# Kernel tuning notes

Measured on AMD Instinct MI355X. Metric: run time of the kernel, lower is better.

## Reference

```python
import jax, jax.numpy as jnp
import numpy as np

INPUT_DIM = 1024
OUTPUT_DIM = 1024
DOWN = INPUT_DIM // 8  # reduction_factor=8
NUM_TOKENS = 2


def setup_inputs() -> dict:
    key = jax.random.key(0)
    k1, k2, k3, k4, k5 = jax.random.split(key, 5)
    B, Sx, Sy = 32, 2048, 512
    x = jax.random.normal(k1, (B, Sx, INPUT_DIM), dtype=jnp.float32)
    y = jax.random.normal(k2, (B, Sy, INPUT_DIM), dtype=jnp.float32)
    # nn.Parameter(torch.rand(...)) -> uniform [0,1)
    latent_tokens = jax.random.uniform(k3, (NUM_TOKENS, INPUT_DIM), dtype=jnp.float32)
    gate = jnp.zeros((1,), dtype=jnp.float32)
    # Conv1d kernel_size=1, no bias == pointwise matmul; kaiming-uniform-ish init
    lim_d = 1.0 / np.sqrt(INPUT_DIM)
    lim_u = 1.0 / np.sqrt(DOWN)
    W_down = jax.random.uniform(k4, (DOWN, INPUT_DIM), dtype=jnp.float32, minval=-lim_d, maxval=lim_d)
    W_up = jax.random.uniform(k5, (OUTPUT_DIM, DOWN), dtype=jnp.float32, minval=-lim_u, maxval=lim_u)
    return {"x": x, "y": y, "latent_tokens": latent_tokens, "gate": gate,
            "W_down": W_down, "W_up": W_up}


def reference(x, y, latent_tokens, gate, W_down, W_up):
    # tokens attend over y:  [B,T,Sy] softmax over Sy
    att_y2t = jax.nn.softmax(jnp.einsum('td,bsd->bts', latent_tokens, y), axis=-1)
    tokens = latent_tokens[None] + jnp.einsum('bts,bsd->btd', att_y2t, y)  # [B,T,D]
    # x attends over tokens: [B,Sx,T] softmax over T
    att_t2x = jax.nn.softmax(jnp.einsum('bsd,btd->bst', x, tokens), axis=-1)
    x_res = jnp.einsum('bst,btd->bsd', att_t2x, tokens)
    x = x + gate * x_res
    # 1x1 conv bottleneck: down -> ReLU -> up (pointwise matmuls)
    z = jax.nn.relu(jnp.einsum('bsd,ed->bse', x, W_down))
    out = jnp.einsum('bse,oe->bso', z, W_up)
    return out
```

## Files before the change

### kernel.cpp

```cpp
#include <hip/hip_runtime.h>
#include <hip/hip_bf16.h>

#define B_N 32
#define SX 2048
#define SY 512
#define DIM 1024
#define NTOK 2
#define DN 128
#define ODIM 1024
#define BM 64
#define KH 512

typedef __bf16 bf16;
typedef __bf16 bf16x8 __attribute__((ext_vector_type(8)));
typedef __bf16 bf16x4 __attribute__((ext_vector_type(4)));
typedef float f32x4 __attribute__((ext_vector_type(4)));

__device__ __forceinline__ f32x4 mfma16(bf16x8 a, bf16x8 b, f32x4 c) {
  return __builtin_amdgcn_mfma_f32_16x16x32_bf16(a, b, c, 0, 0, 0);
}

__global__ __launch_bounds__(256) void prep_kernel(const float* __restrict__ Wd,
                                                   const float* __restrict__ Wu,
                                                   bf16* __restrict__ wdb,
                                                   bf16* __restrict__ wub) {
  int i = blockIdx.x * 256 + threadIdx.x;
  if (i < DN * DIM) {
    wdb[i] = (bf16)Wd[i];
    wub[i] = (bf16)Wu[i];
  }
}

__global__ __launch_bounds__(256) void tokens_kernel(const float* __restrict__ y,
                                                     const float* __restrict__ lat,
                                                     const float* __restrict__ gate,
                                                     float* __restrict__ tokens) {
  if (gate[0] == 0.0f) return;
  __shared__ float s_lat[NTOK][DIM];
  __shared__ float s_sc[NTOK][SY];
  int b = blockIdx.x;
  int tid = threadIdx.x, wave = tid >> 6, lane = tid & 63;
  const float* yb = y + (size_t)b * SY * DIM;
  for (int i = tid; i < NTOK * DIM; i += 256) ((float*)s_lat)[i] = lat[i];
  __syncthreads();
  for (int s = wave * 128; s < wave * 128 + 128; ++s) {
    const float* yr = yb + (size_t)s * DIM;
    float d0 = 0.f, d1 = 0.f;
#pragma unroll
    for (int i = 0; i < 4; ++i) {
      f32x4 v = *(const f32x4*)(yr + lane * 4 + i * 256);
      f32x4 l0 = *(const f32x4*)(&s_lat[0][lane * 4 + i * 256]);
      f32x4 l1 = *(const f32x4*)(&s_lat[1][lane * 4 + i * 256]);
      d0 += v[0] * l0[0] + v[1] * l0[1] + v[2] * l0[2] + v[3] * l0[3];
      d1 += v[0] * l1[0] + v[1] * l1[1] + v[2] * l1[2] + v[3] * l1[3];
    }
#pragma unroll
    for (int off = 32; off > 0; off >>= 1) {
      d0 += __shfl_xor(d0, off);
      d1 += __shfl_xor(d1, off);
    }
    if (lane == 0) { s_sc[0][s] = d0; s_sc[1][s] = d1; }
  }
  __syncthreads();
  if (wave < 2) {
    float m = -3.4e38f;
    for (int s = lane; s < SY; s += 64) m = fmaxf(m, s_sc[wave][s]);
#pragma unroll
    for (int off = 32; off > 0; off >>= 1) m = fmaxf(m, __shfl_xor(m, off));
    float sum = 0.f;
    for (int s = lane; s < SY; s += 64) {
      float e = expf(s_sc[wave][s] - m);
      s_sc[wave][s] = e;
      sum += e;
    }
#pragma unroll
    for (int off = 32; off > 0; off >>= 1) sum += __shfl_xor(sum, off);
    float inv = 1.f / sum;
    for (int s = lane; s < SY; s += 64) s_sc[wave][s] *= inv;
  }
  __syncthreads();
  float a0[4] = {0.f, 0.f, 0.f, 0.f}, a1[4] = {0.f, 0.f, 0.f, 0.f};
  for (int s = 0; s < SY; ++s) {
    float p0 = s_sc[0][s], p1 = s_sc[1][s];
    const float* yr = yb + (size_t)s * DIM;
#pragma unroll
    for (int i = 0; i < 4; ++i) {
      float v = yr[tid + i * 256];
      a0[i] += p0 * v;
      a1[i] += p1 * v;
    }
  }
  float* tb = tokens + (size_t)b * NTOK * DIM;
#pragma unroll
  for (int i = 0; i < 4; ++i) {
    tb[tid + i * 256] = s_lat[0][tid + i * 256] + a0[i];
    tb[DIM + tid + i * 256] = s_lat[1][tid + i * 256] + a1[i];
  }
}

__global__ __launch_bounds__(256) void xprime_kernel(const float* __restrict__ x,
                                                     const float* __restrict__ gate,
                                                     const float* __restrict__ tokens,
                                                     float* __restrict__ xp) {
  float g = gate[0];
  if (g == 0.0f) return;
  __shared__ float s_tok[NTOK][DIM];
  __shared__ float s_c[BM][2];
  int tid = threadIdx.x, w = tid >> 6, lane = tid & 63;
  size_t m0 = (size_t)blockIdx.x * BM;
  int b = (int)(m0 / SX);
  const float* xb = x + m0 * DIM;
  const float* tokb = tokens + (size_t)b * NTOK * DIM;
  for (int i = tid; i < NTOK * DIM; i += 256) ((float*)s_tok)[i] = tokb[i];
  __syncthreads();
  for (int i = 0; i < 16; ++i) {
    int r = w * 16 + i;
    const float* xrow = xb + (size_t)r * DIM;
    float d0 = 0.f, d1 = 0.f;
#pragma unroll
    for (int c = 0; c < 4; ++c) {
      f32x4 v = *(const f32x4*)(xrow + lane * 4 + c * 256);
      f32x4 t0 = *(const f32x4*)(&s_tok[0][lane * 4 + c * 256]);
      f32x4 t1 = *(const f32x4*)(&s_tok[1][lane * 4 + c * 256]);
      d0 += v[0] * t0[0] + v[1] * t0[1] + v[2] * t0[2] + v[3] * t0[3];
      d1 += v[0] * t1[0] + v[1] * t1[1] + v[2] * t1[2] + v[3] * t1[3];
    }
#pragma unroll
    for (int off = 32; off > 0; off >>= 1) {
      d0 += __shfl_xor(d0, off);
      d1 += __shfl_xor(d1, off);
    }
    if (lane == 0) {
      float mm = fmaxf(d0, d1);
      float e0 = expf(d0 - mm), e1 = expf(d1 - mm);
      float inv = g / (e0 + e1);
      s_c[r][0] = e0 * inv;
      s_c[r][1] = e1 * inv;
    }
  }
  __syncthreads();
  float* xpb = xp + m0 * DIM;
  for (int r = w * 16; r < w * 16 + 16; ++r) {
    float c0 = s_c[r][0], c1 = s_c[r][1];
#pragma unroll
    for (int c = 0; c < 4; ++c) {
      f32x4 v = *(const f32x4*)(xb + (size_t)r * DIM + lane * 4 + c * 256);
      f32x4 t0 = *(const f32x4*)(&s_tok[0][lane * 4 + c * 256]);
      f32x4 t1 = *(const f32x4*)(&s_tok[1][lane * 4 + c * 256]);
      f32x4 o;
#pragma unroll
      for (int j = 0; j < 4; ++j) o[j] = v[j] + c0 * t0[j] + c1 * t1[j];
      *(f32x4*)(xpb + (size_t)r * DIM + lane * 4 + c * 256) = o;
    }
  }
}

__global__ __launch_bounds__(512, 4) void main_kernel(const float* __restrict__ x,
                                                      const float* __restrict__ gate,
                                                      const float* __restrict__ xp,
                                                      const bf16* __restrict__ wdb,
                                                      const bf16* __restrict__ wub,
                                                      float* __restrict__ out) {
  __shared__ bf16 xs[BM * KH];
  __shared__ bf16 zsm[BM * DN];

  int tid = threadIdx.x, w = tid >> 6, lane = tid & 63;
  int lq = lane >> 4, lr = lane & 15;
  size_t m0 = (size_t)blockIdx.x * BM;
  float g = gate[0];
  const float* xb = ((g != 0.f) ? xp : x) + m0 * DIM;

  char* xls = (char*)xs;
  char* zls = (char*)zsm;

  f32x4 acc[4] = {};

  auto LOADH = [&](int h) {
    f32x4 xv[8][2];
#pragma unroll
    for (int i = 0; i < 8; ++i) {
      int row = w + i * 8;
      const float* p = xb + (size_t)row * DIM + h * KH + lane * 8;
      xv[i][0] = *(const f32x4*)p;
      xv[i][1] = *(const f32x4*)(p + 4);
    }
#pragma unroll
    for (int i = 0; i < 8; ++i) {
      int row = w + i * 8;
      bf16x8 o;
#pragma unroll
      for (int j = 0; j < 4; ++j) {
        o[j] = (bf16)xv[i][0][j];
        o[4 + j] = (bf16)xv[i][1][j];
      }
      *(bf16x8*)(xls + row * (KH * 2) + ((lane * 16) ^ (w << 4))) = o;
    }
  };

  auto COMPH = [&](int h) {
    const bf16* wdw = wdb + (size_t)(w * 16 + lr) * DIM + h * KH + lq * 8;
#pragma unroll 4
    for (int kc = 0; kc < KH / 32; ++kc) {
      bf16x8 wf = *(const bf16x8*)(wdw + kc * 32);
#pragma unroll
      for (int mt = 0; mt < 4; ++mt) {
        int xr = mt * 16 + lr;
        bf16x8 xf = *(const bf16x8*)(xls + xr * (KH * 2) +
                                     (((kc * 32 + lq * 8) * 2) ^ ((xr & 7) << 4)));
        acc[mt] = mfma16(wf, xf, acc[mt]);
      }
    }
  };

  LOADH(0);
  __syncthreads();
  COMPH(0);
  __syncthreads();
  LOADH(1);
  __syncthreads();
  COMPH(1);

#pragma unroll
  for (int mt = 0; mt < 4; ++mt) {
    int xr = mt * 16 + lr;
    int dn = w * 16 + lq * 4;
    bf16x4 pk;
#pragma unroll
    for (int r = 0; r < 4; ++r) pk[r] = (bf16)fmaxf(acc[mt][r], 0.f);
    *(bf16x4*)(zls + xr * (DN * 2) + ((dn * 2) ^ ((xr & 7) << 4))) = pk;
  }
  __syncthreads();

  bf16x8 zF[4][4];
#pragma unroll
  for (int mt = 0; mt < 4; ++mt)
#pragma unroll
    for (int kt = 0; kt < 4; ++kt) {
      int xr = mt * 16 + lr;
      zF[kt][mt] = *(const bf16x8*)(zls + xr * (DN * 2) +
                                    (((kt * 32 + lq * 8) * 2) ^ ((xr & 7) << 4)));
    }

  float* ob = out + m0 * ODIM;
#pragma unroll 2
  for (int oc16 = 0; oc16 < 8; ++oc16) {
    int base = w * 128 + oc16 * 16;
    bf16x8 wu[4];
#pragma unroll
    for (int kt = 0; kt < 4; ++kt)
      wu[kt] = *(const bf16x8*)(wub + (size_t)(base + lr) * DN + kt * 32 + lq * 8);
    f32x4 a2[4] = {};
#pragma unroll
    for (int kt = 0; kt < 4; ++kt)
#pragma unroll
      for (int mt = 0; mt < 4; ++mt)
        a2[mt] = mfma16(wu[kt], zF[kt][mt], a2[mt]);
#pragma unroll
    for (int mt = 0; mt < 4; ++mt)
      *(f32x4*)(ob + (size_t)(mt * 16 + lr) * ODIM + base + lq * 4) = a2[mt];
  }
}

extern "C" void kernel_launch(void* const* d_in, const int* in_sizes, int n_in,
                              void* d_out, int out_size, void* d_ws, size_t ws_size,
                              hipStream_t stream) {
  const float* x = (const float*)d_in[0];
  const float* y = (const float*)d_in[1];
  const float* lat = (const float*)d_in[2];
  const float* gate = (const float*)d_in[3];
  const float* Wd = (const float*)d_in[4];
  const float* Wu = (const float*)d_in[5];
  float* out = (float*)d_out;
  char* ws = (char*)d_ws;

  float* tokens = (float*)ws;
  bf16* wdb = (bf16*)(ws + 262144);
  bf16* wub = (bf16*)(ws + 524288);

  prep_kernel<<<(DN * DIM + 255) / 256, 256, 0, stream>>>(Wd, Wu, wdb, wub);
  tokens_kernel<<<B_N, 256, 0, stream>>>(y, lat, gate, tokens);
  xprime_kernel<<<(B_N * SX) / BM, 256, 0, stream>>>(x, gate, tokens, out);
  main_kernel<<<(B_N * SX) / BM, 512, 0, stream>>>(x, gate, out, wdb, wub, out);
}
```

Before: 162.6 us.

## Double-buffer x tiles in LDS and prefetch next K-quarter into registers

Splits the down-projection K loop into four 256-wide quarters with two LDS buffers. Global loads of the next x quarter and the W_down fragments are issued into registers before the MFMAs on the current buffer run, so load latency overlaps compute. The old scheme loaded half of K, synced, then computed with no overlap. The cost is more registers for the prefetched data, extra barriers per quarter, and a rewritten LDS swizzle that the read and write sides must agree on.

```diff
diff --git a/kernel.cpp b/kernel.cpp
--- a/kernel.cpp
+++ b/kernel.cpp
@@ -9,7 +9,8 @@
 #define DN 128
 #define ODIM 1024
 #define BM 64
-#define KH 512
+#define QK 256
+#define NQ 4
 
 typedef __bf16 bf16;
 typedef __bf16 bf16x8 __attribute__((ext_vector_type(8)));
@@ -161,7 +162,7 @@
                                                       const bf16* __restrict__ wdb,
                                                       const bf16* __restrict__ wub,
                                                       float* __restrict__ out) {
-  __shared__ bf16 xs[BM * KH];
+  __shared__ bf16 xq[2][BM * QK];
   __shared__ bf16 zsm[BM * DN];
 
   int tid = threadIdx.x, w = tid >> 6, lane = tid & 63;
@@ -170,55 +171,74 @@
   float g = gate[0];
   const float* xb = ((g != 0.f) ? xp : x) + m0 * DIM;
 
-  char* xls = (char*)xs;
+  int srow = tid >> 5;
+  int scolb = (tid & 31) * 16;
+  const float* xgp = xb + (size_t)srow * DIM + (tid & 31) * 8;
+
+  f32x4 xs0[4], xs1[4];
+  bf16x8 wdr[8];
+  f32x4 acc[4] = {};
+
+  const bf16* wdp = wdb + (size_t)(w * 16 + lr) * DIM + lq * 8;
+
+  char* xls = (char*)xq;
   char* zls = (char*)zsm;
 
-  f32x4 acc[4] = {};
-
-  auto LOADH = [&](int h) {
-    f32x4 xv[8][2];
-#pragma unroll
-    for (int i = 0; i < 8; ++i) {
-      int row = w + i * 8;
-      const float* p = xb + (size_t)row * DIM + h * KH + lane * 8;
-      xv[i][0] = *(const f32x4*)p;
-      xv[i][1] = *(const f32x4*)(p + 4);
-    }
-#pragma unroll
-    for (int i = 0; i < 8; ++i) {
-      int row = w + i * 8;
+  auto XLOAD = [&](int q) {
+#pragma unroll
+    for (int i = 0; i < 4; ++i) {
+      const float* p = xgp + (size_t)i * 16 * DIM + q * QK;
+      xs0[i] = *(const f32x4*)p;
+      xs1[i] = *(const f32x4*)(p + 4);
+    }
+  };
+  auto WLOAD = [&](int q) {
+#pragma unroll
+    for (int kc = 0; kc < 8; ++kc)
+      wdr[kc] = *(const bf16x8*)(wdp + q * QK + kc * 32);
+  };
+  auto XWRITE = [&](int buf) {
+    char* base = xls + buf * (BM * QK * 2);
+#pragma unroll
+    for (int i = 0; i < 4; ++i) {
+      int row = i * 16 + srow;
       bf16x8 o;
 #pragma unroll
       for (int j = 0; j < 4; ++j) {
-        o[j] = (bf16)xv[i][0][j];
-        o[4 + j] = (bf16)xv[i][1][j];
+        o[j] = (bf16)xs0[i][j];
+        o[4 + j] = (bf16)xs1[i][j];
       }
-      *(bf16x8*)(xls + row * (KH * 2) + ((lane * 16) ^ (w << 4))) = o;
+      *(bf16x8*)(base + row * (QK * 2) + (scolb ^ ((row & 7) << 4))) = o;
     }
   };
-
-  auto COMPH = [&](int h) {
-    const bf16* wdw = wdb + (size_t)(w * 16 + lr) * DIM + h * KH + lq * 8;
-#pragma unroll 4
-    for (int kc = 0; kc < KH / 32; ++kc) {
-      bf16x8 wf = *(const bf16x8*)(wdw + kc * 32);
+  auto COMP = [&](int buf) {
+    const char* base = xls + buf * (BM * QK * 2);
+#pragma unroll
+    for (int kc = 0; kc < 8; ++kc) {
 #pragma unroll
       for (int mt = 0; mt < 4; ++mt) {
-        int xr = mt * 16 + lr;
-        bf16x8 xf = *(const bf16x8*)(xls + xr * (KH * 2) +
-                                     (((kc * 32 + lq * 8) * 2) ^ ((xr & 7) << 4)));
-        acc[mt] = mfma16(wf, xf, acc[mt]);
+        int row = mt * 16 + lr;
+        bf16x8 xf = *(const bf16x8*)(base + row * (QK * 2) +
+                                     ((kc * 64 + lq * 16) ^ ((row & 7) << 4)));
+        acc[mt] = mfma16(wdr[kc], xf, acc[mt]);
       }
     }
   };
 
-  LOADH(0);
-  __syncthreads();
-  COMPH(0);
-  __syncthreads();
-  LOADH(1);
-  __syncthreads();
-  COMPH(1);
+  XLOAD(0);
+  WLOAD(0);
+  XWRITE(0);
+  __syncthreads();
+
+#pragma unroll
+  for (int q = 0; q < NQ; ++q) {
+    if (q + 1 < NQ) XLOAD(q + 1);
+    COMP(q & 1);
+    if (q + 1 < NQ) WLOAD(q + 1);
+    __syncthreads();
+    if (q + 1 < NQ) XWRITE((q + 1) & 1);
+    __syncthreads();
+  }
 
 #pragma unroll
   for (int mt = 0; mt < 4; ++mt) {
```

New measurement: 159.7 us. Within noise of the previous version (-1.8%).

## Pipeline down-projection GEMM with a 3-stage global_load_lds ring buffer

Applied to the files above, without the earlier changes.

Replaces the two-half load-then-compute scheme for the down-projection with a 16-step K loop. It uses a 3-deep LDS ring filled by direct global-to-LDS copies of fp32 x tiles and bf16 W_down tiles, with manual vmcnt waits and barriers. Conversion of x to bf16 now happens when fragments are read from LDS, not before they are stored. The aim is to overlap HBM loads of x with MFMA work and to stop stalling on register-staged conversion. The cost is a larger shared-memory footprint (112 KB), which limits the kernel to one block per CU, plus extra conversion work inside the inner loop.

```diff
diff --git a/kernel.cpp b/kernel.cpp
--- a/kernel.cpp
+++ b/kernel.cpp
@@ -9,15 +9,23 @@
 #define DN 128
 #define ODIM 1024
 #define BM 64
-#define KH 512
+#define BK 64
+#define NT 16
+#define RING 3
 
 typedef __bf16 bf16;
 typedef __bf16 bf16x8 __attribute__((ext_vector_type(8)));
 typedef __bf16 bf16x4 __attribute__((ext_vector_type(4)));
 typedef float f32x4 __attribute__((ext_vector_type(4)));
 
+typedef __attribute__((address_space(3))) unsigned char lds_u8;
+typedef const __attribute__((address_space(1))) unsigned char glb_u8;
+
 __device__ __forceinline__ f32x4 mfma16(bf16x8 a, bf16x8 b, f32x4 c) {
   return __builtin_amdgcn_mfma_f32_16x16x32_bf16(a, b, c, 0, 0, 0);
+}
+__device__ __forceinline__ void gll16(const void* g, void* l) {
+  __builtin_amdgcn_global_load_lds((glb_u8*)g, (lds_u8*)l, 16, 0, 0);
 }
 
 __global__ __launch_bounds__(256) void prep_kernel(const float* __restrict__ Wd,
@@ -155,71 +163,94 @@
   }
 }
 
-__global__ __launch_bounds__(512, 4) void main_kernel(const float* __restrict__ x,
-                                                      const float* __restrict__ gate,
-                                                      const float* __restrict__ xp,
-                                                      const bf16* __restrict__ wdb,
-                                                      const bf16* __restrict__ wub,
-                                                      float* __restrict__ out) {
-  __shared__ bf16 xs[BM * KH];
-  __shared__ bf16 zsm[BM * DN];
-
-  int tid = threadIdx.x, w = tid >> 6, lane = tid & 63;
-  int lq = lane >> 4, lr = lane & 15;
+__global__ __launch_bounds__(512) void main_kernel(const float* __restrict__ x,
+                                                   const float* __restrict__ gate,
+                                                   const float* __restrict__ xp,
+                                                   const bf16* __restrict__ wdb,
+                                                   const bf16* __restrict__ wub,
+                                                   float* __restrict__ out) {
+  __shared__ __align__(16) char smem[114688];
+
+  int tid = threadIdx.x, w = tid >> 6, l = tid & 63;
+  int lq = l >> 4, lr = l & 15;
   size_t m0 = (size_t)blockIdx.x * BM;
   float g = gate[0];
   const float* xb = ((g != 0.f) ? xp : x) + m0 * DIM;
 
-  char* xls = (char*)xs;
-  char* zls = (char*)zsm;
+  const char* xsrc[2];
+  const char* wsrc[2];
+#pragma unroll
+  for (int j = 0; j < 2; ++j) {
+    int xr = w * 8 + j * 4 + (l >> 4);
+    int xcb = ((l & 15) * 16) ^ ((j * 4 + (l >> 4)) << 5);
+    xsrc[j] = (const char*)xb + (size_t)xr * (DIM * 4) + xcb;
+    int wr_ = w * 16 + j * 8 + (l >> 3);
+    int wcb = ((l & 7) * 16) ^ ((l >> 3) << 4);
+    wsrc[j] = (const char*)wdb + (size_t)wr_ * (DIM * 2) + wcb;
+  }
 
   f32x4 acc[4] = {};
 
-  auto LOADH = [&](int h) {
-    f32x4 xv[8][2];
-#pragma unroll
-    for (int i = 0; i < 8; ++i) {
-      int row = w + i * 8;
-      const float* p = xb + (size_t)row * DIM + h * KH + lane * 8;
-      xv[i][0] = *(const f32x4*)p;
-      xv[i][1] = *(const f32x4*)(p + 4);
-    }
-#pragma unroll
-    for (int i = 0; i < 8; ++i) {
-      int row = w + i * 8;
-      bf16x8 o;
-#pragma unroll
-      for (int j = 0; j < 4; ++j) {
-        o[j] = (bf16)xv[i][0][j];
-        o[4 + j] = (bf16)xv[i][1][j];
+  auto STAGE = [&](int t) {
+    int b = t % RING;
+#pragma unroll
+    for (int j = 0; j < 2; ++j)
+      gll16(xsrc[j] + (size_t)t * (BK * 4),
+            smem + b * 16384 + (w * 8 + j * 4) * 256);
+#pragma unroll
+    for (int j = 0; j < 2; ++j)
+      gll16(wsrc[j] + (size_t)t * (BK * 2),
+            smem + 49152 + b * 16384 + (w * 16 + j * 8) * 128);
+  };
+
+  auto COMP = [&](int b) {
+    const char* xt = smem + b * 16384;
+    const char* wt = smem + 49152 + b * 16384;
+#pragma unroll
+    for (int kc = 0; kc < 2; ++kc) {
+      int dn = w * 16 + lr;
+      bf16x8 wdf = *(const bf16x8*)(wt + dn * 128 +
+                                    ((kc * 64 + lq * 16) ^ ((lr & 7) << 4)));
+#pragma unroll
+      for (int mt = 0; mt < 4; ++mt) {
+        int row = mt * 16 + lr;
+        int sz = (row & 7) << 5;
+        int kb = kc * 128 + lq * 32;
+        f32x4 a0 = *(const f32x4*)(xt + row * 256 + (kb ^ sz));
+        f32x4 a1 = *(const f32x4*)(xt + row * 256 + ((kb + 16) ^ sz));
+        bf16x8 xf;
+#pragma unroll
+        for (int jj = 0; jj < 4; ++jj) {
+          xf[jj] = (bf16)a0[jj];
+          xf[4 + jj] = (bf16)a1[jj];
+        }
+        acc[mt] = mfma16(wdf, xf, acc[mt]);
       }
-      *(bf16x8*)(xls + row * (KH * 2) + ((lane * 16) ^ (w << 4))) = o;
     }
   };
 
-  auto COMPH = [&](int h) {
-    const bf16* wdw = wdb + (size_t)(w * 16 + lr) * DIM + h * KH + lq * 8;
-#pragma unroll 4
-    for (int kc = 0; kc < KH / 32; ++kc) {
-      bf16x8 wf = *(const bf16x8*)(wdw + kc * 32);
-#pragma unroll
-      for (int mt = 0; mt < 4; ++mt) {
-        int xr = mt * 16 + lr;
-        bf16x8 xf = *(const bf16x8*)(xls + xr * (KH * 2) +
-                                     (((kc * 32 + lq * 8) * 2) ^ ((xr & 7) << 4)));
-        acc[mt] = mfma16(wf, xf, acc[mt]);
-      }
-    }
-  };
-
-  LOADH(0);
-  __syncthreads();
-  COMPH(0);
-  __syncthreads();
-  LOADH(1);
-  __syncthreads();
-  COMPH(1);
-
+  STAGE(0);
+  STAGE(1);
+  STAGE(2);
+
+#pragma unroll
+  for (int t = 0; t < NT; ++t) {
+    if (t > 0 && t + 2 < NT) STAGE(t + 2);
+    if (t + 2 < NT) {
+      asm volatile("s_waitcnt vmcnt(8)" ::: "memory");
+    } else if (t == NT - 2) {
+      asm volatile("s_waitcnt vmcnt(4)" ::: "memory");
+    } else {
+      asm volatile("s_waitcnt vmcnt(0)" ::: "memory");
+    }
+    __builtin_amdgcn_sched_barrier(0);
+    __builtin_amdgcn_s_barrier();
+    COMP(t % RING);
+    __builtin_amdgcn_sched_barrier(0);
+    __builtin_amdgcn_s_barrier();
+  }
+
+  char* zls = smem + 98304;
 #pragma unroll
   for (int mt = 0; mt < 4; ++mt) {
     int xr = mt * 16 + lr;
```

Result: faster. 146.0 us (-10.2%).
